# Kernel tuning notes

Measured on AMD Instinct MI355X. Metric: run time of the kernel, lower is better.

Reference implementation:

```python
import jax, jax.numpy as jnp
import numpy as np

N_NODES = 50000
N_EDGES = 1600000
IN_FEATS = 256
N_HEADS = 4
OUT_FEATS = 64
NEG_SLOPE = 0.2  # DGL GATConv default negative_slope


def setup_inputs() -> dict:
    key = jax.random.key(0)
    ks = jax.random.split(key, 8)
    x = jax.random.normal(ks[0], (N_NODES, IN_FEATS), dtype=jnp.float32)
    src = jax.random.randint(ks[1], (N_EDGES,), 0, N_NODES)
    dst = jax.random.randint(ks[2], (N_EDGES,), 0, N_NODES)
    # learned params (DGL GATConv: fc weight, attn_l, attn_r, bias)
    scale = 1.0 / np.sqrt(IN_FEATS)
    W = jax.random.normal(ks[3], (IN_FEATS, N_HEADS * OUT_FEATS), dtype=jnp.float32) * scale
    attn_l = jax.random.normal(ks[4], (N_HEADS, OUT_FEATS), dtype=jnp.float32) * 0.1
    attn_r = jax.random.normal(ks[5], (N_HEADS, OUT_FEATS), dtype=jnp.float32) * 0.1
    bias = jnp.zeros((N_HEADS * OUT_FEATS,), dtype=jnp.float32)
    return {"x": x, "src": src, "dst": dst, "W": W, "attn_l": attn_l, "attn_r": attn_r, "bias": bias}


def reference(x, src, dst, W, attn_l, attn_r, bias):
    N = x.shape[0]
    H, D = attn_l.shape
    # linear projection, split into heads: [N, H, D]
    feat = (x @ W).reshape(N, H, D)
    # per-node attention halves: [N, H]
    el = (feat * attn_l[None]).sum(-1)
    er = (feat * attn_r[None]).sum(-1)
    # per-edge unnormalized scores: [E, H]
    e = jax.nn.leaky_relu(el[src] + er[dst], negative_slope=NEG_SLOPE)
    # segment softmax over incoming edges of each destination node
    m = jax.ops.segment_max(e, dst, num_segments=N)  # [N, H]
    m = jnp.where(jnp.isfinite(m), m, 0.0)  # nodes with no in-edges
    ex = jnp.exp(e - m[dst])
    s = jax.ops.segment_sum(ex, dst, num_segments=N)  # [N, H]
    alpha = ex / s[dst]  # [E, H]
    # weighted scatter-aggregate of source features: [N, H, D]
    msg = feat[src] * alpha[..., None]
    out = jax.ops.segment_sum(msg, dst, num_segments=N)
    out = out + bias.reshape(1, H, D)
    # last_layer=False -> flatten heads
    return out.reshape(N, H * D)
```

## Files before the change

kernel.cpp:

```cpp
#include <hip/hip_runtime.h>
#include <math.h>

#define HEADS 4
#define DH 64
#define HD 256
#define INF_ 256
#define NEG 0.2f
#define CAP 128

typedef __attribute__((ext_vector_type(8))) __bf16 bf16x8;
typedef __attribute__((ext_vector_type(4))) float f32x4;

__device__ __forceinline__ float lrelu(float v) { return v >= 0.0f ? v : NEG * v; }

__device__ __forceinline__ unsigned short f2bf(float f) {
    unsigned u = __float_as_uint(f);
    u += 0x7fffu + ((u >> 16) & 1u);
    return (unsigned short)(u >> 16);
}

__device__ void prep_w_body(const float* __restrict__ W, unsigned short* __restrict__ wfrag,
                            int bid) {
    int t = bid * 256 + threadIdx.x;
    if (t >= 16 * 8 * 64) return;
    int lane = t & 63;
    int ks = (t >> 6) & 7;
    int ct = t >> 9;
    int col = ct * 16 + (lane & 15);
    int k0 = ks * 32 + (lane >> 4) * 8;
    ushort4 lo, hi;
    lo.x = f2bf(W[(size_t)(k0 + 0) * HD + col]);
    lo.y = f2bf(W[(size_t)(k0 + 1) * HD + col]);
    lo.z = f2bf(W[(size_t)(k0 + 2) * HD + col]);
    lo.w = f2bf(W[(size_t)(k0 + 3) * HD + col]);
    hi.x = f2bf(W[(size_t)(k0 + 4) * HD + col]);
    hi.y = f2bf(W[(size_t)(k0 + 5) * HD + col]);
    hi.z = f2bf(W[(size_t)(k0 + 6) * HD + col]);
    hi.w = f2bf(W[(size_t)(k0 + 7) * HD + col]);
    *(ushort4*)(wfrag + (size_t)t * 8) = lo;
    *(ushort4*)(wfrag + (size_t)t * 8 + 4) = hi;
}

__global__ __launch_bounds__(256) void prep_zero_kernel(
    const float* __restrict__ W, unsigned short* __restrict__ wfrag,
    int* __restrict__ cur, int N) {
    if ((int)blockIdx.x < 32) {
        prep_w_body(W, wfrag, blockIdx.x);
    } else {
        int i = ((int)blockIdx.x - 32) * 256 + (int)threadIdx.x;
        if (i < N) cur[i] = 0;
    }
}


__device__ void scatter_body(const int* __restrict__ src, const int* __restrict__ dst,
                             int* __restrict__ cur, int* __restrict__ csr_src,
                             int E, int N, int bid, int nbg) {
    int g = bid & 7;
    int bi = bid >> 3;
    int RS = (N + 7) >> 3;
    int lo = g * RS;
    int hi = min(N, lo + RS);
    int tid = bi * 256 + (int)threadIdx.x;
    int stride = nbg * 256;
    const int4* d4 = (const int4*)dst;
    int e4 = E >> 2;
    for (int i = tid; i < e4; i += stride) {
        int4 v = d4[i];
        if (v.x >= lo && v.x < hi) { int p = atomicAdd(&cur[v.x], 1); csr_src[(size_t)v.x * CAP + p] = src[i * 4 + 0]; }
        if (v.y >= lo && v.y < hi) { int p = atomicAdd(&cur[v.y], 1); csr_src[(size_t)v.y * CAP + p] = src[i * 4 + 1]; }
        if (v.z >= lo && v.z < hi) { int p = atomicAdd(&cur[v.z], 1); csr_src[(size_t)v.z * CAP + p] = src[i * 4 + 2]; }
        if (v.w >= lo && v.w < hi) { int p = atomicAdd(&cur[v.w], 1); csr_src[(size_t)v.w * CAP + p] = src[i * 4 + 3]; }
    }
    if (tid < (E & 3)) {
        int e = e4 * 4 + tid;
        int v = dst[e];
        if (v >= lo && v < hi) { int p = atomicAdd(&cur[v], 1); csr_src[(size_t)v * CAP + p] = src[e]; }
    }
}

#define ASTRIDE 264
__device__ void gemm_body(const float* __restrict__ x, const unsigned short* __restrict__ wfrag,
                          const float* __restrict__ attn_l, const float* __restrict__ attn_r,
                          unsigned short* __restrict__ feat16, float* __restrict__ el,
                          float* __restrict__ er, int N, int bid) {
    __shared__ __align__(16) unsigned short As[64 * ASTRIDE];
    int tid = threadIdx.x;
    int row0 = bid * 64;
    {
        const float4* xg = (const float4*)(x + (size_t)row0 * INF_);
#pragma unroll
        for (int j = 0; j < 16; ++j) {
            int flat = j * 256 + tid;
            int r = flat >> 6;
            int c4 = flat & 63;
            float4 v = make_float4(0, 0, 0, 0);
            if (row0 + r < N) v = xg[(size_t)r * 64 + c4];
            ushort4 b;
            b.x = f2bf(v.x); b.y = f2bf(v.y); b.z = f2bf(v.z); b.w = f2bf(v.w);
            *(ushort4*)(As + r * ASTRIDE + c4 * 4) = b;
        }
    }
    __syncthreads();

    int lane = tid & 63;
    int w = tid >> 6;
    int lm = lane & 15;
    int hi = lane >> 4;

    f32x4 acc[4][4];
#pragma unroll
    for (int a = 0; a < 4; ++a)
#pragma unroll
        for (int b = 0; b < 4; ++b) acc[a][b] = (f32x4)0.0f;

    const bf16x8* wf = (const bf16x8*)wfrag;
#pragma unroll
    for (int ks = 0; ks < 8; ++ks) {
        bf16x8 afr[4], bfr[4];
#pragma unroll
        for (int rt = 0; rt < 4; ++rt)
            afr[rt] = *(const bf16x8*)(As + (rt * 16 + lm) * ASTRIDE + ks * 32 + hi * 8);
#pragma unroll
        for (int ct = 0; ct < 4; ++ct)
            bfr[ct] = wf[(size_t)((w * 4 + ct) * 8 + ks) * 64 + lane];
#pragma unroll
        for (int rt = 0; rt < 4; ++rt)
#pragma unroll
            for (int ct = 0; ct < 4; ++ct)
                acc[rt][ct] = __builtin_amdgcn_mfma_f32_16x16x32_bf16(afr[rt], bfr[ct], acc[rt][ct], 0, 0, 0);
    }

    float al[4], ar[4];
#pragma unroll
    for (int ct = 0; ct < 4; ++ct) {
        al[ct] = attn_l[w * DH + ct * 16 + lm];
        ar[ct] = attn_r[w * DH + ct * 16 + lm];
    }
#pragma unroll
    for (int rt = 0; rt < 4; ++rt) {
#pragma unroll
        for (int r = 0; r < 4; ++r) {
            int row = row0 + rt * 16 + hi * 4 + r;
            bool ok = row < N;
            float pl = 0.0f, pr = 0.0f;
#pragma unroll
            for (int ct = 0; ct < 4; ++ct) {
                float v = acc[rt][ct][r];
                pl += v * al[ct];
                pr += v * ar[ct];
                if (ok) feat16[(size_t)row * HD + w * DH + ct * 16 + lm] = f2bf(v);
            }
#pragma unroll
            for (int off = 1; off < 16; off <<= 1) {
                pl += __shfl_xor(pl, off);
                pr += __shfl_xor(pr, off);
            }
            if (ok && lm == 0) {
                el[(size_t)row * 4 + w] = pl;
                er[(size_t)row * 4 + w] = pr;
            }
        }
    }
}

__global__ __launch_bounds__(256) void scatter_gemm_kernel(
    const int* __restrict__ src, const int* __restrict__ dst,
    int* __restrict__ cur, int* __restrict__ csr_src,
    const float* __restrict__ x, const unsigned short* __restrict__ wfrag,
    const float* __restrict__ attn_l, const float* __restrict__ attn_r,
    unsigned short* __restrict__ feat16, float* __restrict__ el,
    float* __restrict__ er, int E, int N, int nScat) {
    if ((int)blockIdx.x < nScat)
        scatter_body(src, dst, cur, csr_src, E, N, blockIdx.x, nScat >> 3);
    else
        gemm_body(x, wfrag, attn_l, attn_r, feat16, el, er, N, blockIdx.x - nScat);
}


__global__ __launch_bounds__(256) void node_aggregate_kernel(
    const int* __restrict__ cur, const int* __restrict__ csr_src,
    const float* __restrict__ el, const float* __restrict__ er,
    const unsigned short* __restrict__ feat16, const float* __restrict__ bias,
    float* __restrict__ out, int N) {
    int lane = threadIdx.x & 63;
    int node = blockIdx.x * 4 + (threadIdx.x >> 6);
    if (node >= N) return;
    int hw = lane & 3;
    int hc = lane >> 4;
    int coff = lane * 4;
    int r0 = node * CAP;
    int deg = cur[node];
    int r1 = r0 + deg;
    float er_w = er[(size_t)node * 4 + hw];
    float s_part = 0.0f;
    float4 acc = make_float4(0, 0, 0, 0);

    int pFull = r0 + (deg & ~15);

#define WPHASE(P0)                                                        \
    int eidx = (P0) + (lane >> 2);                                        \
    bool valid = eidx < r1;                                               \
    int sn_l = valid ? csr_src[eidx] : 0;                                 \
    float elv = el[sn_l * 4 + hw];                                        \
    float w_l = valid ? __expf(lrelu(elv + er_w)) : 0.0f;                 \
    s_part += w_l;

#define FEDGE(E)                                                          \
    {                                                                     \
        float w_e = __shfl(w_l, (E) * 4 + hc);                            \
        int sn_e = __shfl(sn_l, (E) * 4);                                 \
        uint2 uu = *(const uint2*)(feat16 + (unsigned)(sn_e * HD + coff));\
        acc.x += w_e * __uint_as_float(uu.x << 16);                       \
        acc.y += w_e * __uint_as_float(uu.x & 0xffff0000u);               \
        acc.z += w_e * __uint_as_float(uu.y << 16);                       \
        acc.w += w_e * __uint_as_float(uu.y & 0xffff0000u);               \
    }

    for (int p0 = r0; p0 < pFull; p0 += 16) {
        WPHASE(p0)
#pragma unroll
        for (int e = 0; e < 16; ++e) FEDGE(e)
    }
    if (pFull < r1) {
        WPHASE(pFull)
        int nT = r1 - pFull;
        for (int e = 0; e < nT; ++e) FEDGE(e)
    }
#undef WPHASE
#undef FEDGE

#pragma unroll
    for (int off = 4; off < 64; off <<= 1) s_part += __shfl_xor(s_part, off);
    float s_h = __shfl(s_part, hc);
    float rs = (deg > 0) ? 1.0f / s_h : 0.0f;

    float4 b4 = *(const float4*)(bias + coff);
    float4 o;
    o.x = acc.x * rs + b4.x;
    o.y = acc.y * rs + b4.y;
    o.z = acc.z * rs + b4.z;
    o.w = acc.w * rs + b4.w;
    *(float4*)(out + (size_t)node * HD + coff) = o;
}

extern "C" void kernel_launch(void* const* d_in, const int* in_sizes, int n_in,
                              void* d_out, int out_size, void* d_ws, size_t ws_size,
                              hipStream_t stream) {
    const float* x = (const float*)d_in[0];
    const int* src = (const int*)d_in[1];
    const int* dst = (const int*)d_in[2];
    const float* W = (const float*)d_in[3];
    const float* attn_l = (const float*)d_in[4];
    const float* attn_r = (const float*)d_in[5];
    const float* bias = (const float*)d_in[6];
    float* out = (float*)d_out;
    int N = in_sizes[0] / INF_;
    int E = in_sizes[1];

    unsigned short* feat16 = (unsigned short*)d_ws;
    unsigned short* wfrag = feat16 + (size_t)N * HD;
    float* el = (float*)(wfrag + 16 * 8 * 64 * 8);
    float* er = el + (size_t)N * HEADS;
    int* cur = (int*)(er + (size_t)N * HEADS);
    int* csr_src = cur + N;

    const int nScat = 1024;
    int nGemm = (N + 63) / 64;
    int nZero = (N + 255) / 256;

    prep_zero_kernel<<<32 + nZero, 256, 0, stream>>>(W, wfrag, cur, N);
    scatter_gemm_kernel<<<nScat + nGemm, 256, 0, stream>>>(src, dst, cur, csr_src,
                                                           x, wfrag, attn_l, attn_r,
                                                           feat16, el, er, E, N, nScat);
    node_aggregate_kernel<<<(N + 3) / 4, 256, 0, stream>>>(cur, csr_src, el, er,
                                                           feat16, bias, out, N);
}
```

Before: 219.7 us.

## Restructure launches: memset counters, fuse weight prep with scatter, separate GEMM kernel

Counter zeroing moves to hipMemsetAsync, and the weight-fragment prep is merged into the CSR scatter kernel. The bf16 MFMA GEMM now runs as its own kernel after the scatter, where before it shared a launch with the scatter. The scatter loads src as int4 vectors and its block count doubles. This removes the earlier overlap of scatter and GEMM inside one launch, trading it for a simpler schedule and fewer scalar loads, and it still uses the same number of launches plus a memset.

```diff
diff --git a/kernel.cpp b/kernel.cpp
--- a/kernel.cpp
+++ b/kernel.cpp
@@ -18,6 +18,7 @@
     u += 0x7fffu + ((u >> 16) & 1u);
     return (unsigned short)(u >> 16);
 }
+
 
 __device__ void prep_w_body(const float* __restrict__ W, unsigned short* __restrict__ wfrag,
                             int bid) {
@@ -41,18 +42,6 @@
     *(ushort4*)(wfrag + (size_t)t * 8 + 4) = hi;
 }
 
-__global__ __launch_bounds__(256) void prep_zero_kernel(
-    const float* __restrict__ W, unsigned short* __restrict__ wfrag,
-    int* __restrict__ cur, int N) {
-    if ((int)blockIdx.x < 32) {
-        prep_w_body(W, wfrag, blockIdx.x);
-    } else {
-        int i = ((int)blockIdx.x - 32) * 256 + (int)threadIdx.x;
-        if (i < N) cur[i] = 0;
-    }
-}
-
-
 __device__ void scatter_body(const int* __restrict__ src, const int* __restrict__ dst,
                              int* __restrict__ cur, int* __restrict__ csr_src,
                              int E, int N, int bid, int nbg) {
@@ -64,13 +53,15 @@
     int tid = bi * 256 + (int)threadIdx.x;
     int stride = nbg * 256;
     const int4* d4 = (const int4*)dst;
+    const int4* s4 = (const int4*)src;
     int e4 = E >> 2;
     for (int i = tid; i < e4; i += stride) {
         int4 v = d4[i];
-        if (v.x >= lo && v.x < hi) { int p = atomicAdd(&cur[v.x], 1); csr_src[(size_t)v.x * CAP + p] = src[i * 4 + 0]; }
-        if (v.y >= lo && v.y < hi) { int p = atomicAdd(&cur[v.y], 1); csr_src[(size_t)v.y * CAP + p] = src[i * 4 + 1]; }
-        if (v.z >= lo && v.z < hi) { int p = atomicAdd(&cur[v.z], 1); csr_src[(size_t)v.z * CAP + p] = src[i * 4 + 2]; }
-        if (v.w >= lo && v.w < hi) { int p = atomicAdd(&cur[v.w], 1); csr_src[(size_t)v.w * CAP + p] = src[i * 4 + 3]; }
+        int4 s = s4[i];
+        if (v.x >= lo && v.x < hi) { int p = atomicAdd(&cur[v.x], 1); csr_src[(size_t)v.x * CAP + p] = s.x; }
+        if (v.y >= lo && v.y < hi) { int p = atomicAdd(&cur[v.y], 1); csr_src[(size_t)v.y * CAP + p] = s.y; }
+        if (v.z >= lo && v.z < hi) { int p = atomicAdd(&cur[v.z], 1); csr_src[(size_t)v.z * CAP + p] = s.z; }
+        if (v.w >= lo && v.w < hi) { int p = atomicAdd(&cur[v.w], 1); csr_src[(size_t)v.w * CAP + p] = s.w; }
     }
     if (tid < (E & 3)) {
         int e = e4 * 4 + tid;
@@ -79,14 +70,25 @@
     }
 }
 
+__global__ __launch_bounds__(256) void prep_scatter_kernel(
+    const float* __restrict__ W, unsigned short* __restrict__ wfrag,
+    const int* __restrict__ src, const int* __restrict__ dst,
+    int* __restrict__ cur, int* __restrict__ csr_src, int E, int N, int nScat) {
+    if ((int)blockIdx.x < 32)
+        prep_w_body(W, wfrag, blockIdx.x);
+    else
+        scatter_body(src, dst, cur, csr_src, E, N, (int)blockIdx.x - 32, nScat >> 3);
+}
+
 #define ASTRIDE 264
-__device__ void gemm_body(const float* __restrict__ x, const unsigned short* __restrict__ wfrag,
-                          const float* __restrict__ attn_l, const float* __restrict__ attn_r,
-                          unsigned short* __restrict__ feat16, float* __restrict__ el,
-                          float* __restrict__ er, int N, int bid) {
+__global__ __launch_bounds__(256) void gemm_mfma_kernel(
+    const float* __restrict__ x, const unsigned short* __restrict__ wfrag,
+    const float* __restrict__ attn_l, const float* __restrict__ attn_r,
+    unsigned short* __restrict__ feat16, float* __restrict__ el,
+    float* __restrict__ er, int N) {
     __shared__ __align__(16) unsigned short As[64 * ASTRIDE];
     int tid = threadIdx.x;
-    int row0 = bid * 64;
+    int row0 = blockIdx.x * 64;
     {
         const float4* xg = (const float4*)(x + (size_t)row0 * INF_);
 #pragma unroll
@@ -162,19 +164,6 @@
             }
         }
     }
-}
-
-__global__ __launch_bounds__(256) void scatter_gemm_kernel(
-    const int* __restrict__ src, const int* __restrict__ dst,
-    int* __restrict__ cur, int* __restrict__ csr_src,
-    const float* __restrict__ x, const unsigned short* __restrict__ wfrag,
-    const float* __restrict__ attn_l, const float* __restrict__ attn_r,
-    unsigned short* __restrict__ feat16, float* __restrict__ el,
-    float* __restrict__ er, int E, int N, int nScat) {
-    if ((int)blockIdx.x < nScat)
-        scatter_body(src, dst, cur, csr_src, E, N, blockIdx.x, nScat >> 3);
-    else
-        gemm_body(x, wfrag, attn_l, attn_r, feat16, el, er, N, blockIdx.x - nScat);
 }
 
 
@@ -265,14 +254,14 @@
     int* cur = (int*)(er + (size_t)N * HEADS);
     int* csr_src = cur + N;
 
-    const int nScat = 1024;
+    const int nScat = 2048;
     int nGemm = (N + 63) / 64;
-    int nZero = (N + 255) / 256;
-
-    prep_zero_kernel<<<32 + nZero, 256, 0, stream>>>(W, wfrag, cur, N);
-    scatter_gemm_kernel<<<nScat + nGemm, 256, 0, stream>>>(src, dst, cur, csr_src,
-                                                           x, wfrag, attn_l, attn_r,
-                                                           feat16, el, er, E, N, nScat);
+
+    hipMemsetAsync(cur, 0, (size_t)N * sizeof(int), stream);
+    prep_scatter_kernel<<<32 + nScat, 256, 0, stream>>>(W, wfrag, src, dst, cur,
+                                                        csr_src, E, N, nScat);
+    gemm_mfma_kernel<<<nGemm, 256, 0, stream>>>(x, wfrag, attn_l, attn_r,
+                                                feat16, el, er, N);
     node_aggregate_kernel<<<(N + 3) / 4, 256, 0, stream>>>(cur, csr_src, el, er,
                                                            feat16, bias, out, N);
 }
```

New measurement: 239.1 us. 8.8% more time.
